# Performance work log

Hardware: AMD Instinct MI355X
Metric: run time of the kernel (lower is better)

Reference implementation:

```python
import jax, jax.numpy as jnp
import numpy as np

N = 50000
E = 625000
D = 128
L = 3
BN_EPS = 1e-5


def setup_inputs() -> dict:
    key = jax.random.key(0)
    ks = jax.random.split(key, 12)
    x = jax.random.normal(ks[0], (N, D), dtype=jnp.float32)
    edge_index = jax.random.randint(ks[1], (2, E), 0, N, dtype=jnp.int64)
    s = 1.0 / np.sqrt(D)
    W1 = jax.random.uniform(ks[2], (L, D, D), jnp.float32, -s, s)
    b1 = jax.random.uniform(ks[3], (L, D), jnp.float32, -s, s)
    W2 = jax.random.uniform(ks[4], (L, D, D), jnp.float32, -s, s)
    b2 = jax.random.uniform(ks[5], (L, D), jnp.float32, -s, s)
    eps = jnp.zeros((L,), jnp.float32)  # GINConv train_eps init 0
    gamma = jnp.ones((L, D), jnp.float32)
    beta = jnp.zeros((L, D), jnp.float32)
    Wl = jax.random.uniform(ks[6], (L, D, D), jnp.float32, -s, s)
    bl = jax.random.uniform(ks[7], (L, D), jnp.float32, -s, s)
    return {"x": x, "edge_index": edge_index, "W1": W1, "b1": b1, "W2": W2,
            "b2": b2, "eps": eps, "gamma": gamma, "beta": beta, "Wl": Wl, "bl": bl}


def reference(x, edge_index, W1, b1, W2, b2, eps, gamma, beta, Wl, bl):
    src, dst = edge_index[0], edge_index[1]
    xs = [x]
    h = x
    for i in range(L):
        # GIN aggregation: sum of neighbor (source) features at target nodes
        agg = jax.ops.segment_sum(h[src], dst, num_segments=N)  # [N, D]
        z = (1.0 + eps[i]) * h + agg
        # MLP: Linear -> ReLU -> Linear
        z = jax.nn.relu(z @ W1[i] + b1[i]) @ W2[i] + b2[i]
        # BatchNorm1d (training mode: batch stats, biased variance)
        mu = jnp.mean(z, axis=0)
        var = jnp.mean((z - mu) ** 2, axis=0)
        z = gamma[i] * (z - mu) * jax.lax.rsqrt(var + BN_EPS) + beta[i]
        if i != 0:
            z = z + xs[-1]
        h = jax.nn.relu(z)
        xs.append(h)
    outs = [xs[i + 1] @ Wl[i] + bl[i] for i in range(L)]
    return jnp.concatenate(outs, axis=-1)  # [N, L*D]
```

## Files before the change

### kernel.cpp

```cpp
#include <hip/hip_runtime.h>
#include <hip/hip_bf16.h>
#include <stdint.h>

#define NN 50000
#define NE 625000
#define DD 128
#define NL 3
#define GB 391

typedef __bf16 bf16x8 __attribute__((ext_vector_type(8)));
typedef float f32x4 __attribute__((ext_vector_type(4)));

__device__ __forceinline__ float bflo(uint32_t u) { return __uint_as_float(u << 16); }
__device__ __forceinline__ float bfhi(uint32_t u) { return __uint_as_float(u & 0xffff0000u); }
__device__ __forceinline__ uint16_t f2bf(float f) {
    __hip_bfloat16 h = __float2bfloat16(f);
    return __builtin_bit_cast(uint16_t, h);
}
__device__ __forceinline__ uint32_t pack2(float lo, float hi) {
    return (uint32_t)f2bf(lo) | ((uint32_t)f2bf(hi) << 16);
}

__global__ void k_hist(const int* __restrict__ dstv, int* __restrict__ deg) {
    int e = blockIdx.x * 256 + threadIdx.x;
    if (e < NE) atomicAdd(&deg[dstv[e]], 1);
}

__global__ __launch_bounds__(512) void k_bsum(const int* __restrict__ deg, int* __restrict__ bsum) {
    __shared__ int s[512];
    int i = blockIdx.x * 512 + threadIdx.x;
    int v = (i < NN) ? deg[i] : 0;
    s[threadIdx.x] = v;
    __syncthreads();
    for (int st = 256; st > 0; st >>= 1) {
        if (threadIdx.x < st) s[threadIdx.x] += s[threadIdx.x + st];
        __syncthreads();
    }
    if (threadIdx.x == 0) bsum[blockIdx.x] = s[0];
}

__global__ __launch_bounds__(128) void k_scanbs(const int* __restrict__ bsum, int* __restrict__ bsoff) {
    __shared__ int s[128];
    int t = threadIdx.x;
    int v = (t < 98) ? bsum[t] : 0;
    s[t] = v;
    __syncthreads();
    for (int st = 1; st < 128; st <<= 1) {
        int a = (t >= st) ? s[t - st] : 0;
        __syncthreads();
        s[t] += a;
        __syncthreads();
    }
    if (t < 98) bsoff[t] = s[t] - v;
}

__global__ __launch_bounds__(512) void k_scan2(int* __restrict__ deg_cursor,
                                               const int* __restrict__ bsoff,
                                               int* __restrict__ rowptr) {
    __shared__ int s[512];
    int t = threadIdx.x;
    int i = blockIdx.x * 512 + t;
    int v = (i < NN) ? deg_cursor[i] : 0;
    s[t] = v;
    __syncthreads();
    for (int st = 1; st < 512; st <<= 1) {
        int a = (t >= st) ? s[t - st] : 0;
        __syncthreads();
        s[t] += a;
        __syncthreads();
    }
    if (i < NN) {
        int excl = bsoff[blockIdx.x] + s[t] - v;
        rowptr[i] = excl;
        deg_cursor[i] = excl;
        if (i == NN - 1) rowptr[NN] = excl + v;
    }
}

__global__ void k_fill(const int* __restrict__ srcv, const int* __restrict__ dstv,
                       int* __restrict__ cursor, int* __restrict__ colv) {
    int e = blockIdx.x * 256 + threadIdx.x;
    if (e < NE) {
        int d = dstv[e];
        int p = atomicAdd(&cursor[d], 1);
        colv[p] = srcv[e];
    }
}

__global__ void k_convert_w(const float* __restrict__ W1, const float* __restrict__ W2,
                            const float* __restrict__ Wl, uint16_t* __restrict__ Wb) {
    int id = blockIdx.x * 256 + threadIdx.x;
    if (id >= 9 * 16384) return;
    int m = id >> 14;
    int r = id & 16383;
    int k = r >> 7;
    int col = r & 127;
    const float* src;
    if (m < 3) src = W1 + m * 16384;
    else if (m < 6) src = W2 + (m - 3) * 16384;
    else src = Wl + (m - 6) * 16384;
    float v = src[k * 128 + col];
    Wb[m * 16384 + col * 128 + (k ^ ((col & 7) << 3))] = f2bf(v);
}

__global__ void k_x2bf(const float* __restrict__ x, uint16_t* __restrict__ hb,
                       int* __restrict__ cursor) {
    int id = blockIdx.x * 256 + threadIdx.x;
    if (id < NN) cursor[id] = 0;
    int base = id * 4;
    if (base >= NN * DD) return;
    float4 v = *(const float4*)(x + base);
    uint2 st;
    st.x = pack2(v.x, v.y);
    st.y = pack2(v.z, v.w);
    *(uint2*)(hb + base) = st;
}

__global__ __launch_bounds__(256) void k_agg(const uint16_t* __restrict__ hb,
                                             const int* __restrict__ rowptr,
                                             const int* __restrict__ colv,
                                             const float* __restrict__ epsp, int layer,
                                             uint16_t* __restrict__ zb,
                                             float* __restrict__ bnsum) {
    if (blockIdx.x == 0) bnsum[threadIdx.x] = 0.f;
    int g = (blockIdx.x * 256 + threadIdx.x) >> 4;
    int l16 = threadIdx.x & 15;
    if (g >= NN) return;
    float onepe = 1.0f + epsp[layer];
    int beg = rowptr[g], end = rowptr[g + 1];
    const uint4* hp = (const uint4*)hb;
    float a0 = 0.f, a1 = 0.f, a2 = 0.f, a3 = 0.f, a4 = 0.f, a5 = 0.f, a6 = 0.f, a7 = 0.f;
    int j = beg;
    for (; j + 3 < end; j += 4) {
        int s0 = colv[j];
        int s1 = colv[j + 1];
        int s2 = colv[j + 2];
        int s3 = colv[j + 3];
        uint4 u0 = hp[(size_t)s0 * 16 + l16];
        uint4 u1 = hp[(size_t)s1 * 16 + l16];
        uint4 u2 = hp[(size_t)s2 * 16 + l16];
        uint4 u3 = hp[(size_t)s3 * 16 + l16];
        a0 += bflo(u0.x); a1 += bfhi(u0.x); a2 += bflo(u0.y); a3 += bfhi(u0.y);
        a4 += bflo(u0.z); a5 += bfhi(u0.z); a6 += bflo(u0.w); a7 += bfhi(u0.w);
        a0 += bflo(u1.x); a1 += bfhi(u1.x); a2 += bflo(u1.y); a3 += bfhi(u1.y);
        a4 += bflo(u1.z); a5 += bfhi(u1.z); a6 += bflo(u1.w); a7 += bfhi(u1.w);
        a0 += bflo(u2.x); a1 += bfhi(u2.x); a2 += bflo(u2.y); a3 += bfhi(u2.y);
        a4 += bflo(u2.z); a5 += bfhi(u2.z); a6 += bflo(u2.w); a7 += bfhi(u2.w);
        a0 += bflo(u3.x); a1 += bfhi(u3.x); a2 += bflo(u3.y); a3 += bfhi(u3.y);
        a4 += bflo(u3.z); a5 += bfhi(u3.z); a6 += bflo(u3.w); a7 += bfhi(u3.w);
    }
    for (; j < end; ++j) {
        int s0 = colv[j];
        uint4 u = hp[(size_t)s0 * 16 + l16];
        a0 += bflo(u.x); a1 += bfhi(u.x); a2 += bflo(u.y); a3 += bfhi(u.y);
        a4 += bflo(u.z); a5 += bfhi(u.z); a6 += bflo(u.w); a7 += bfhi(u.w);
    }
    uint4 hu = hp[(size_t)g * 16 + l16];
    a0 = fmaf(onepe, bflo(hu.x), a0); a1 = fmaf(onepe, bfhi(hu.x), a1);
    a2 = fmaf(onepe, bflo(hu.y), a2); a3 = fmaf(onepe, bfhi(hu.y), a3);
    a4 = fmaf(onepe, bflo(hu.z), a4); a5 = fmaf(onepe, bfhi(hu.z), a5);
    a6 = fmaf(onepe, bflo(hu.w), a6); a7 = fmaf(onepe, bfhi(hu.w), a7);
    uint4 st;
    st.x = pack2(a0, a1); st.y = pack2(a2, a3);
    st.z = pack2(a4, a5); st.w = pack2(a6, a7);
    ((uint4*)zb)[(size_t)g * 16 + l16] = st;
}

__global__ __launch_bounds__(256) void k_mlp(const uint16_t* __restrict__ A,
                                             const uint16_t* __restrict__ W1img,
                                             const uint16_t* __restrict__ W2img,
                                             const float* __restrict__ b1,
                                             const float* __restrict__ b2,
                                             float* __restrict__ bnsum,
                                             float* __restrict__ z2) {
    __shared__ uint16_t ldsW[16384];
    __shared__ uint16_t ldsT[16384];
    int tid = threadIdx.x;
    int wid = tid >> 6, lane = tid & 63;

    bf16x8 w2r[8];
#pragma unroll
    for (int it = 0; it < 8; ++it) w2r[it] = *(const bf16x8*)(W2img + (it * 256 + tid) * 8);

#pragma unroll
    for (int it = 0; it < 8; ++it) {
        int idx = (it * 256 + tid) * 8;
        *(bf16x8*)(&ldsW[idx]) = *(const bf16x8*)(W1img + idx);
    }
    __syncthreads();

    const int brow = blockIdx.x * 128;
    const int m0 = wid * 32;
    const int l15 = lane & 15;
    const int lhi = lane >> 4;

    f32x4 acc[2][8];
    f32x4 zero = {0.f, 0.f, 0.f, 0.f};
#pragma unroll
    for (int m = 0; m < 2; ++m)
#pragma unroll
        for (int n = 0; n < 8; ++n) acc[m][n] = zero;

    const char* Ab = (const char*)A;
#pragma unroll
    for (int kk = 0; kk < 4; ++kk) {
        int kbyte = kk * 64 + (lhi << 4);
        bf16x8 afrag[2];
#pragma unroll
        for (int m = 0; m < 2; ++m) {
            int row = brow + m0 + m * 16 + l15;
            if (row >= NN) row = NN - 1;
            afrag[m] = *(const bf16x8*)(Ab + (size_t)row * 256 + kbyte);
        }
#pragma unroll
        for (int n = 0; n < 8; ++n) {
            int col = n * 16 + l15;
            int addr = col * 256 + (kbyte ^ ((col & 7) << 4));
            bf16x8 bfrag = *(const bf16x8*)((const char*)ldsW + addr);
            acc[0][n] = __builtin_amdgcn_mfma_f32_16x16x32_bf16(afrag[0], bfrag, acc[0][n], 0, 0, 0);
            acc[1][n] = __builtin_amdgcn_mfma_f32_16x16x32_bf16(afrag[1], bfrag, acc[1][n], 0, 0, 0);
        }
    }

    {
        float bc[8];
#pragma unroll
        for (int n = 0; n < 8; ++n) bc[n] = b1[n * 16 + l15];
#pragma unroll
        for (int m = 0; m < 2; ++m) {
            int rbase = m0 + m * 16 + (lhi << 2);
#pragma unroll
            for (int r = 0; r < 4; ++r) {
                int row = rbase + r;
#pragma unroll
                for (int n = 0; n < 8; ++n) {
                    float v = fmaxf(acc[m][n][r] + bc[n], 0.f);
                    int col = n * 16 + l15;
                    int byteoff = row * 256 + ((col * 2) ^ ((row & 7) << 4));
                    *(uint16_t*)((char*)ldsT + byteoff) = f2bf(v);
                }
            }
        }
    }
    __syncthreads();

#pragma unroll
    for (int it = 0; it < 8; ++it) *(bf16x8*)(&ldsW[(it * 256 + tid) * 8]) = w2r[it];
    __syncthreads();

#pragma unroll
    for (int m = 0; m < 2; ++m)
#pragma unroll
        for (int n = 0; n < 8; ++n) acc[m][n] = zero;

#pragma unroll
    for (int kk = 0; kk < 4; ++kk) {
        int kbyte = kk * 64 + (lhi << 4);
        bf16x8 afrag[2];
#pragma unroll
        for (int m = 0; m < 2; ++m) {
            int rowl = m0 + m * 16 + l15;
            afrag[m] = *(const bf16x8*)((const char*)ldsT + rowl * 256 + (kbyte ^ ((rowl & 7) << 4)));
        }
#pragma unroll
        for (int n = 0; n < 8; ++n) {
            int col = n * 16 + l15;
            int addr = col * 256 + (kbyte ^ ((col & 7) << 4));
            bf16x8 bfrag = *(const bf16x8*)((const char*)ldsW + addr);
            acc[0][n] = __builtin_amdgcn_mfma_f32_16x16x32_bf16(afrag[0], bfrag, acc[0][n], 0, 0, 0);
            acc[1][n] = __builtin_amdgcn_mfma_f32_16x16x32_bf16(afrag[1], bfrag, acc[1][n], 0, 0, 0);
        }
    }

    float bc2[8];
#pragma unroll
    for (int n = 0; n < 8; ++n) bc2[n] = b2[n * 16 + l15];

    float s1[8], s2[8];
#pragma unroll
    for (int n = 0; n < 8; ++n) { s1[n] = 0.f; s2[n] = 0.f; }

#pragma unroll
    for (int m = 0; m < 2; ++m) {
        int rbase = brow + m0 + m * 16 + (lhi << 2);
#pragma unroll
        for (int r = 0; r < 4; ++r) {
            int row = rbase + r;
            bool ok = row < NN;
#pragma unroll
            for (int n = 0; n < 8; ++n) {
                float v = acc[m][n][r] + bc2[n];
                if (ok) {
                    z2[(size_t)row * 128 + n * 16 + l15] = v;
                    s1[n] += v;
                    s2[n] += v * v;
                }
            }
        }
    }

    __syncthreads();
    float* ls = (float*)ldsT;
    ls[tid] = 0.f;
    __syncthreads();
#pragma unroll
    for (int n = 0; n < 8; ++n) {
        float a1 = s1[n] + __shfl_xor(s1[n], 16);
        a1 += __shfl_xor(a1, 32);
        float a2 = s2[n] + __shfl_xor(s2[n], 16);
        a2 += __shfl_xor(a2, 32);
        if (lane < 16) {
            atomicAdd(&ls[n * 16 + lane], a1);
            atomicAdd(&ls[128 + n * 16 + lane], a2);
        }
    }
    __syncthreads();
    atomicAdd(&bnsum[tid], ls[tid]);
}

__global__ __launch_bounds__(256) void k_apply(const float* __restrict__ z2,
                                               const uint16_t* __restrict__ hin,
                                               const float* __restrict__ bnsum,
                                               const float* __restrict__ gamma,
                                               const float* __restrict__ beta, int layer,
                                               uint16_t* __restrict__ hout) {
    __shared__ float sA[128], sB[128];
    int tid = threadIdx.x;
    if (tid < 128) {
        float mu = bnsum[tid] * (1.0f / NN);
        float var = bnsum[128 + tid] * (1.0f / NN) - mu * mu;
        float a = gamma[layer * 128 + tid] * rsqrtf(var + 1e-5f);
        sA[tid] = a;
        sB[tid] = beta[layer * 128 + tid] - mu * a;
    }
    __syncthreads();
    int id = blockIdx.x * 256 + tid;
    int base = id * 4;
    if (base >= NN * DD) return;
    int c = base & 127;
    float4 z = *(const float4*)(z2 + base);
    float4 av = *(const float4*)(sA + c);
    float4 bv = *(const float4*)(sB + c);
    float v0 = fmaf(av.x, z.x, bv.x);
    float v1 = fmaf(av.y, z.y, bv.y);
    float v2 = fmaf(av.z, z.z, bv.z);
    float v3 = fmaf(av.w, z.w, bv.w);
    if (layer > 0) {
        uint2 h = *(const uint2*)(hin + base);
        v0 += bflo(h.x);
        v1 += bfhi(h.x);
        v2 += bflo(h.y);
        v3 += bfhi(h.y);
    }
    v0 = fmaxf(v0, 0.f);
    v1 = fmaxf(v1, 0.f);
    v2 = fmaxf(v2, 0.f);
    v3 = fmaxf(v3, 0.f);
    uint2 st;
    st.x = pack2(v0, v1);
    st.y = pack2(v2, v3);
    *(uint2*)(hout + base) = st;
}

__global__ __launch_bounds__(256) void k_outgemm(const uint16_t* __restrict__ h1,
                                                 const uint16_t* __restrict__ h2,
                                                 const uint16_t* __restrict__ h3,
                                                 const uint16_t* __restrict__ Wb6,
                                                 const float* __restrict__ bl,
                                                 float* __restrict__ out) {
    __shared__ uint16_t lds[16384];
    int layer = blockIdx.x / GB;
    int blk = blockIdx.x - layer * GB;
    const uint16_t* A = (layer == 0) ? h1 : ((layer == 1) ? h2 : h3);
    const uint16_t* Wimg = Wb6 + layer * 16384;
    const float* bias = bl + layer * 128;

    int tid = threadIdx.x;
    int wid = tid >> 6, lane = tid & 63;
#pragma unroll
    for (int it = 0; it < 8; ++it) {
        int idx = (it * 256 + tid) * 8;
        bf16x8 v = *(const bf16x8*)(Wimg + idx);
        *(bf16x8*)(&lds[idx]) = v;
    }
    __syncthreads();

    const int brow = blk * 128;
    const int m0 = wid * 32;
    const int l15 = lane & 15;
    const int lhi = lane >> 4;

    f32x4 acc[2][8];
    f32x4 zero = {0.f, 0.f, 0.f, 0.f};
#pragma unroll
    for (int m = 0; m < 2; ++m)
#pragma unroll
        for (int n = 0; n < 8; ++n) acc[m][n] = zero;

    const char* Ab = (const char*)A;
#pragma unroll
    for (int kk = 0; kk < 4; ++kk) {
        int kbyte = kk * 64 + (lhi << 4);
        bf16x8 afrag[2];
#pragma unroll
        for (int m = 0; m < 2; ++m) {
            int row = brow + m0 + m * 16 + l15;
            if (row >= NN) row = NN - 1;
            afrag[m] = *(const bf16x8*)(Ab + (size_t)row * 256 + kbyte);
        }
#pragma unroll
        for (int n = 0; n < 8; ++n) {
            int col = n * 16 + l15;
            int addr = col * 256 + (kbyte ^ ((col & 7) << 4));
            bf16x8 bfrag = *(const bf16x8*)((const char*)lds + addr);
            acc[0][n] = __builtin_amdgcn_mfma_f32_16x16x32_bf16(afrag[0], bfrag, acc[0][n], 0, 0, 0);
            acc[1][n] = __builtin_amdgcn_mfma_f32_16x16x32_bf16(afrag[1], bfrag, acc[1][n], 0, 0, 0);
        }
    }

    float bcol[8];
#pragma unroll
    for (int n = 0; n < 8; ++n) bcol[n] = bias[n * 16 + l15];

#pragma unroll
    for (int m = 0; m < 2; ++m) {
        int rbase = brow + m0 + m * 16 + (lhi << 2);
#pragma unroll
        for (int r = 0; r < 4; ++r) {
            int row = rbase + r;
            if (row < NN) {
#pragma unroll
                for (int n = 0; n < 8; ++n) {
                    float v = acc[m][n][r] + bcol[n];
                    out[(size_t)row * (NL * DD) + layer * 128 + n * 16 + l15] = v;
                }
            }
        }
    }
}

extern "C" void kernel_launch(void* const* d_in, const int* in_sizes, int n_in,
                              void* d_out, int out_size, void* d_ws, size_t ws_size,
                              hipStream_t stream) {
    const float* x = (const float*)d_in[0];
    const int* ei = (const int*)d_in[1];
    const float* W1 = (const float*)d_in[2];
    const float* b1 = (const float*)d_in[3];
    const float* W2 = (const float*)d_in[4];
    const float* b2 = (const float*)d_in[5];
    const float* epsp = (const float*)d_in[6];
    const float* gamma = (const float*)d_in[7];
    const float* beta = (const float*)d_in[8];
    const float* Wl = (const float*)d_in[9];
    const float* bl = (const float*)d_in[10];
    float* out = (float*)d_out;

    char* w = (char*)d_ws;
    size_t off = 0;
    auto take = [&](size_t b) -> char* {
        char* p = w + off;
        off += (b + 255) & ~(size_t)255;
        return p;
    };
    uint16_t* hb[4];
    for (int i = 0; i < 4; ++i) hb[i] = (uint16_t*)take((size_t)NN * DD * 2);
    uint16_t* zb = (uint16_t*)take((size_t)NN * DD * 2);
    float* z2 = (float*)take((size_t)NN * DD * 4);
    int* rowptr = (int*)take((size_t)(NN + 1) * 4);
    int* cursor = (int*)take((size_t)NN * 4);
    int* colv = (int*)take((size_t)NE * 4);
    int* bsum = (int*)take(128 * 4);
    int* bsoff = (int*)take(128 * 4);
    uint16_t* Wb = (uint16_t*)take(9 * 16384 * 2);
    float* bnsum = (float*)take(256 * 4);

    const int* srcv = ei;
    const int* dstv = ei + NE;

    k_convert_w<<<(9 * 16384 + 255) / 256, 256, 0, stream>>>(W1, W2, Wl, Wb);
    k_x2bf<<<(NN * DD / 4 + 255) / 256, 256, 0, stream>>>(x, hb[0], cursor);

    k_hist<<<(NE + 255) / 256, 256, 0, stream>>>(dstv, cursor);
    k_bsum<<<98, 512, 0, stream>>>(cursor, bsum);
    k_scanbs<<<1, 128, 0, stream>>>(bsum, bsoff);
    k_scan2<<<98, 512, 0, stream>>>(cursor, bsoff, rowptr);
    k_fill<<<(NE + 255) / 256, 256, 0, stream>>>(srcv, dstv, cursor, colv);

    const int agg_blocks = (NN * 16 + 255) / 256;

    for (int l = 0; l < NL; ++l) {
        k_agg<<<agg_blocks, 256, 0, stream>>>(hb[l], rowptr, colv, epsp, l, zb, bnsum);
        k_mlp<<<GB, 256, 0, stream>>>(zb, Wb + l * 16384, Wb + (3 + l) * 16384,
                                      b1 + l * 128, b2 + l * 128, bnsum, z2);
        k_apply<<<(NN * DD / 4 + 255) / 256, 256, 0, stream>>>(z2, hb[l], bnsum, gamma, beta,
                                                               l, hb[l + 1]);
    }
    k_outgemm<<<NL * GB, 256, 0, stream>>>(hb[1], hb[2], hb[3], Wb + 6 * 16384, bl, out);
}
```

Baseline: 272.6 us.

## Fuse MLP, batchnorm apply and output GEMM into one kernel with grid barrier

```diff
diff --git a/kernel.cpp b/kernel.cpp
--- a/kernel.cpp
+++ b/kernel.cpp
@@ -13,6 +13,7 @@
 
 __device__ __forceinline__ float bflo(uint32_t u) { return __uint_as_float(u << 16); }
 __device__ __forceinline__ float bfhi(uint32_t u) { return __uint_as_float(u & 0xffff0000u); }
+__device__ __forceinline__ float bf1(uint16_t u) { return __uint_as_float(((uint32_t)u) << 16); }
 __device__ __forceinline__ uint16_t f2bf(float f) {
     __hip_bfloat16 h = __float2bfloat16(f);
     return __builtin_bit_cast(uint16_t, h);
@@ -104,8 +105,9 @@
 }
 
 __global__ void k_x2bf(const float* __restrict__ x, uint16_t* __restrict__ hb,
-                       int* __restrict__ cursor) {
+                       int* __restrict__ cursor, int* __restrict__ barcnt) {
     int id = blockIdx.x * 256 + threadIdx.x;
+    if (id == 0) *barcnt = 0;
     if (id < NN) cursor[id] = 0;
     int base = id * 4;
     if (base >= NN * DD) return;
@@ -166,34 +168,36 @@
     ((uint4*)zb)[(size_t)g * 16 + l16] = st;
 }
 
-__global__ __launch_bounds__(256) void k_mlp(const uint16_t* __restrict__ A,
-                                             const uint16_t* __restrict__ W1img,
-                                             const uint16_t* __restrict__ W2img,
-                                             const float* __restrict__ b1,
-                                             const float* __restrict__ b2,
-                                             float* __restrict__ bnsum,
-                                             float* __restrict__ z2) {
+__global__ __launch_bounds__(256, 2) void k_layer(
+    const uint16_t* __restrict__ zb, const uint16_t* __restrict__ hprev,
+    const uint16_t* __restrict__ W1img, const uint16_t* __restrict__ W2img,
+    const uint16_t* __restrict__ Wlimg,
+    const float* __restrict__ b1, const float* __restrict__ b2,
+    const float* __restrict__ blv,
+    const float* __restrict__ gammal, const float* __restrict__ betal,
+    int has_skip, float* __restrict__ bnsum, int* __restrict__ barcnt, int target,
+    uint16_t* __restrict__ hnext, float* __restrict__ outl) {
     __shared__ uint16_t ldsW[16384];
     __shared__ uint16_t ldsT[16384];
+    __shared__ float sAB[256];
+
     int tid = threadIdx.x;
     int wid = tid >> 6, lane = tid & 63;
-
-    bf16x8 w2r[8];
-#pragma unroll
-    for (int it = 0; it < 8; ++it) w2r[it] = *(const bf16x8*)(W2img + (it * 256 + tid) * 8);
-
-#pragma unroll
-    for (int it = 0; it < 8; ++it) {
-        int idx = (it * 256 + tid) * 8;
-        *(bf16x8*)(&ldsW[idx]) = *(const bf16x8*)(W1img + idx);
-    }
-    __syncthreads();
-
     const int brow = blockIdx.x * 128;
     const int m0 = wid * 32;
     const int l15 = lane & 15;
     const int lhi = lane >> 4;
 
+    bf16x8 wpre[8];
+#pragma unroll
+    for (int it = 0; it < 8; ++it) wpre[it] = *(const bf16x8*)(W2img + (it * 256 + tid) * 8);
+#pragma unroll
+    for (int it = 0; it < 8; ++it) {
+        int idx = (it * 256 + tid) * 8;
+        *(bf16x8*)(&ldsW[idx]) = *(const bf16x8*)(W1img + idx);
+    }
+    __syncthreads();
+
     f32x4 acc[2][8];
     f32x4 zero = {0.f, 0.f, 0.f, 0.f};
 #pragma unroll
@@ -201,7 +205,7 @@
 #pragma unroll
         for (int n = 0; n < 8; ++n) acc[m][n] = zero;
 
-    const char* Ab = (const char*)A;
+    const char* Ab = (const char*)zb;
 #pragma unroll
     for (int kk = 0; kk < 4; ++kk) {
         int kbyte = kk * 64 + (lhi << 4);
@@ -245,7 +249,9 @@
     __syncthreads();
 
 #pragma unroll
-    for (int it = 0; it < 8; ++it) *(bf16x8*)(&ldsW[(it * 256 + tid) * 8]) = w2r[it];
+    for (int it = 0; it < 8; ++it) *(bf16x8*)(&ldsW[(it * 256 + tid) * 8]) = wpre[it];
+#pragma unroll
+    for (int it = 0; it < 8; ++it) wpre[it] = *(const bf16x8*)(Wlimg + (it * 256 + tid) * 8);
     __syncthreads();
 
 #pragma unroll
@@ -272,34 +278,50 @@
         }
     }
 
-    float bc2[8];
-#pragma unroll
-    for (int n = 0; n < 8; ++n) bc2[n] = b2[n * 16 + l15];
-
+    {
+        float bc2[8];
+#pragma unroll
+        for (int n = 0; n < 8; ++n) bc2[n] = b2[n * 16 + l15];
+#pragma unroll
+        for (int m = 0; m < 2; ++m)
+#pragma unroll
+            for (int n = 0; n < 8; ++n)
+#pragma unroll
+                for (int r = 0; r < 4; ++r) acc[m][n][r] += bc2[n];
+    }
     float s1[8], s2[8];
 #pragma unroll
     for (int n = 0; n < 8; ++n) { s1[n] = 0.f; s2[n] = 0.f; }
-
 #pragma unroll
     for (int m = 0; m < 2; ++m) {
         int rbase = brow + m0 + m * 16 + (lhi << 2);
 #pragma unroll
         for (int r = 0; r < 4; ++r) {
-            int row = rbase + r;
-            bool ok = row < NN;
-#pragma unroll
-            for (int n = 0; n < 8; ++n) {
-                float v = acc[m][n][r] + bc2[n];
-                if (ok) {
-                    z2[(size_t)row * 128 + n * 16 + l15] = v;
+            bool ok = (rbase + r) < NN;
+            if (ok) {
+#pragma unroll
+                for (int n = 0; n < 8; ++n) {
+                    float v = acc[m][n][r];
                     s1[n] += v;
                     s2[n] += v * v;
                 }
             }
         }
     }
-
-    __syncthreads();
+    __syncthreads();
+
+    {
+        int row = tid >> 1, half = tid & 1;
+        int grow = brow + row;
+        if (grow >= NN) grow = NN - 1;
+        const uint16_t* src = hprev + (size_t)grow * 128;
+#pragma unroll
+        for (int i = 0; i < 8; ++i) {
+            int c = half * 8 + i;
+            uint4 v = *(const uint4*)(src + c * 8);
+            *(uint4*)((char*)ldsW + row * 256 + ((c * 16) ^ ((row & 7) << 4))) = v;
+        }
+    }
     float* ls = (float*)ldsT;
     ls[tid] = 0.f;
     __syncthreads();
@@ -316,112 +338,93 @@
     }
     __syncthreads();
     atomicAdd(&bnsum[tid], ls[tid]);
-}
-
-__global__ __launch_bounds__(256) void k_apply(const float* __restrict__ z2,
-                                               const uint16_t* __restrict__ hin,
-                                               const float* __restrict__ bnsum,
-                                               const float* __restrict__ gamma,
-                                               const float* __restrict__ beta, int layer,
-                                               uint16_t* __restrict__ hout) {
-    __shared__ float sA[128], sB[128];
-    int tid = threadIdx.x;
+    __syncthreads();
+
+    if (tid == 0) {
+        __hip_atomic_fetch_add(barcnt, 1, __ATOMIC_RELEASE, __HIP_MEMORY_SCOPE_AGENT);
+        while (__hip_atomic_load(barcnt, __ATOMIC_ACQUIRE, __HIP_MEMORY_SCOPE_AGENT) < target) {
+            __builtin_amdgcn_s_sleep(2);
+        }
+    }
+    __syncthreads();
+
     if (tid < 128) {
-        float mu = bnsum[tid] * (1.0f / NN);
-        float var = bnsum[128 + tid] * (1.0f / NN) - mu * mu;
-        float a = gamma[layer * 128 + tid] * rsqrtf(var + 1e-5f);
-        sA[tid] = a;
-        sB[tid] = beta[layer * 128 + tid] - mu * a;
-    }
-    __syncthreads();
-    int id = blockIdx.x * 256 + tid;
-    int base = id * 4;
-    if (base >= NN * DD) return;
-    int c = base & 127;
-    float4 z = *(const float4*)(z2 + base);
-    float4 av = *(const float4*)(sA + c);
-    float4 bv = *(const float4*)(sB + c);
-    float v0 = fmaf(av.x, z.x, bv.x);
-    float v1 = fmaf(av.y, z.y, bv.y);
-    float v2 = fmaf(av.z, z.z, bv.z);
-    float v3 = fmaf(av.w, z.w, bv.w);
-    if (layer > 0) {
-        uint2 h = *(const uint2*)(hin + base);
-        v0 += bflo(h.x);
-        v1 += bfhi(h.x);
-        v2 += bflo(h.y);
-        v3 += bfhi(h.y);
-    }
-    v0 = fmaxf(v0, 0.f);
-    v1 = fmaxf(v1, 0.f);
-    v2 = fmaxf(v2, 0.f);
-    v3 = fmaxf(v3, 0.f);
-    uint2 st;
-    st.x = pack2(v0, v1);
-    st.y = pack2(v2, v3);
-    *(uint2*)(hout + base) = st;
-}
-
-__global__ __launch_bounds__(256) void k_outgemm(const uint16_t* __restrict__ h1,
-                                                 const uint16_t* __restrict__ h2,
-                                                 const uint16_t* __restrict__ h3,
-                                                 const uint16_t* __restrict__ Wb6,
-                                                 const float* __restrict__ bl,
-                                                 float* __restrict__ out) {
-    __shared__ uint16_t lds[16384];
-    int layer = blockIdx.x / GB;
-    int blk = blockIdx.x - layer * GB;
-    const uint16_t* A = (layer == 0) ? h1 : ((layer == 1) ? h2 : h3);
-    const uint16_t* Wimg = Wb6 + layer * 16384;
-    const float* bias = bl + layer * 128;
-
-    int tid = threadIdx.x;
-    int wid = tid >> 6, lane = tid & 63;
-#pragma unroll
-    for (int it = 0; it < 8; ++it) {
-        int idx = (it * 256 + tid) * 8;
-        bf16x8 v = *(const bf16x8*)(Wimg + idx);
-        *(bf16x8*)(&lds[idx]) = v;
-    }
-    __syncthreads();
-
-    const int brow = blk * 128;
-    const int m0 = wid * 32;
-    const int l15 = lane & 15;
-    const int lhi = lane >> 4;
-
-    f32x4 acc[2][8];
-    f32x4 zero = {0.f, 0.f, 0.f, 0.f};
+        float su = __hip_atomic_load(&bnsum[tid], __ATOMIC_RELAXED, __HIP_MEMORY_SCOPE_AGENT);
+        float sq = __hip_atomic_load(&bnsum[128 + tid], __ATOMIC_RELAXED, __HIP_MEMORY_SCOPE_AGENT);
+        float mu = su * (1.0f / NN);
+        float var = sq * (1.0f / NN) - mu * mu;
+        float a = gammal[tid] * rsqrtf(var + 1e-5f);
+        sAB[tid] = a;
+        sAB[128 + tid] = betal[tid] - mu * a;
+    }
+    __syncthreads();
+
+#pragma unroll
+    for (int m = 0; m < 2; ++m) {
+        int rbase = m0 + m * 16 + (lhi << 2);
+#pragma unroll
+        for (int r = 0; r < 4; ++r) {
+            int row = rbase + r;
+            int swz = (row & 7) << 4;
+#pragma unroll
+            for (int n = 0; n < 8; ++n) {
+                int col = n * 16 + l15;
+                float v = fmaf(sAB[col], acc[m][n][r], sAB[128 + col]);
+                if (has_skip) {
+                    uint16_t hv = *(const uint16_t*)((const char*)ldsW + row * 256 + ((col * 2) ^ swz));
+                    v += bf1(hv);
+                }
+                v = fmaxf(v, 0.f);
+                *(uint16_t*)((char*)ldsT + row * 256 + ((col * 2) ^ swz)) = f2bf(v);
+            }
+        }
+    }
+    __syncthreads();
+
+    {
+        int row = tid >> 1, half = tid & 1;
+        int grow = brow + row;
+        if (grow < NN) {
+            uint16_t* dst = hnext + (size_t)grow * 128;
+#pragma unroll
+            for (int i = 0; i < 8; ++i) {
+                int c = half * 8 + i;
+                uint4 v = *(const uint4*)((const char*)ldsT + row * 256 + ((c * 16) ^ ((row & 7) << 4)));
+                *(uint4*)(dst + c * 8) = v;
+            }
+        }
+    }
+#pragma unroll
+    for (int it = 0; it < 8; ++it) *(bf16x8*)(&ldsW[(it * 256 + tid) * 8]) = wpre[it];
+    __syncthreads();
+
 #pragma unroll
     for (int m = 0; m < 2; ++m)
 #pragma unroll
         for (int n = 0; n < 8; ++n) acc[m][n] = zero;
 
-    const char* Ab = (const char*)A;
 #pragma unroll
     for (int kk = 0; kk < 4; ++kk) {
         int kbyte = kk * 64 + (lhi << 4);
         bf16x8 afrag[2];
 #pragma unroll
         for (int m = 0; m < 2; ++m) {
-            int row = brow + m0 + m * 16 + l15;
-            if (row >= NN) row = NN - 1;
-            afrag[m] = *(const bf16x8*)(Ab + (size_t)row * 256 + kbyte);
+            int rowl = m0 + m * 16 + l15;
+            afrag[m] = *(const bf16x8*)((const char*)ldsT + rowl * 256 + (kbyte ^ ((rowl & 7) << 4)));
         }
 #pragma unroll
         for (int n = 0; n < 8; ++n) {
             int col = n * 16 + l15;
             int addr = col * 256 + (kbyte ^ ((col & 7) << 4));
-            bf16x8 bfrag = *(const bf16x8*)((const char*)lds + addr);
+            bf16x8 bfrag = *(const bf16x8*)((const char*)ldsW + addr);
             acc[0][n] = __builtin_amdgcn_mfma_f32_16x16x32_bf16(afrag[0], bfrag, acc[0][n], 0, 0, 0);
             acc[1][n] = __builtin_amdgcn_mfma_f32_16x16x32_bf16(afrag[1], bfrag, acc[1][n], 0, 0, 0);
         }
     }
 
-    float bcol[8];
-#pragma unroll
-    for (int n = 0; n < 8; ++n) bcol[n] = bias[n * 16 + l15];
-
+    float bc3[8];
+#pragma unroll
+    for (int n = 0; n < 8; ++n) bc3[n] = blv[n * 16 + l15];
 #pragma unroll
     for (int m = 0; m < 2; ++m) {
         int rbase = brow + m0 + m * 16 + (lhi << 2);
@@ -431,8 +434,7 @@
             if (row < NN) {
 #pragma unroll
                 for (int n = 0; n < 8; ++n) {
-                    float v = acc[m][n][r] + bcol[n];
-                    out[(size_t)row * (NL * DD) + layer * 128 + n * 16 + l15] = v;
+                    outl[(size_t)row * (NL * DD) + n * 16 + l15] = acc[m][n][r] + bc3[n];
                 }
             }
         }
@@ -465,7 +467,6 @@
     uint16_t* hb[4];
     for (int i = 0; i < 4; ++i) hb[i] = (uint16_t*)take((size_t)NN * DD * 2);
     uint16_t* zb = (uint16_t*)take((size_t)NN * DD * 2);
-    float* z2 = (float*)take((size_t)NN * DD * 4);
     int* rowptr = (int*)take((size_t)(NN + 1) * 4);
     int* cursor = (int*)take((size_t)NN * 4);
     int* colv = (int*)take((size_t)NE * 4);
@@ -473,12 +474,13 @@
     int* bsoff = (int*)take(128 * 4);
     uint16_t* Wb = (uint16_t*)take(9 * 16384 * 2);
     float* bnsum = (float*)take(256 * 4);
+    int* barcnt = (int*)take(256);
 
     const int* srcv = ei;
     const int* dstv = ei + NE;
 
     k_convert_w<<<(9 * 16384 + 255) / 256, 256, 0, stream>>>(W1, W2, Wl, Wb);
-    k_x2bf<<<(NN * DD / 4 + 255) / 256, 256, 0, stream>>>(x, hb[0], cursor);
+    k_x2bf<<<(NN * DD / 4 + 255) / 256, 256, 0, stream>>>(x, hb[0], cursor, barcnt);
 
     k_hist<<<(NE + 255) / 256, 256, 0, stream>>>(dstv, cursor);
     k_bsum<<<98, 512, 0, stream>>>(cursor, bsum);
@@ -490,10 +492,11 @@
 
     for (int l = 0; l < NL; ++l) {
         k_agg<<<agg_blocks, 256, 0, stream>>>(hb[l], rowptr, colv, epsp, l, zb, bnsum);
-        k_mlp<<<GB, 256, 0, stream>>>(zb, Wb + l * 16384, Wb + (3 + l) * 16384,
-                                      b1 + l * 128, b2 + l * 128, bnsum, z2);
-        k_apply<<<(NN * DD / 4 + 255) / 256, 256, 0, stream>>>(z2, hb[l], bnsum, gamma, beta,
-                                                               l, hb[l + 1]);
-    }
-    k_outgemm<<<NL * GB, 256, 0, stream>>>(hb[1], hb[2], hb[3], Wb + 6 * 16384, bl, out);
-}
+        k_layer<<<GB, 256, 0, stream>>>(zb, hb[l],
+                                        Wb + l * 16384, Wb + (3 + l) * 16384, Wb + (6 + l) * 16384,
+                                        b1 + l * 128, b2 + l * 128, bl + l * 128,
+                                        gamma + l * 128, beta + l * 128,
+                                        l > 0 ? 1 : 0, bnsum, barcnt, (l + 1) * GB,
+                                        hb[l + 1], out + l * 128);
+    }
+}
```

After: 310.3 us. 13.8% more time.
